# Performance work log

Hardware: AMD Instinct MI355X
Metric: run time of the kernel (lower is better)

## Reference

```python
import jax, jax.numpy as jnp
import numpy as np

B, N, F_IN, F_OUT, E = 2, 8192, 64, 64, 262144
ALPHA = 0.2  # LeakyReLU negative slope


def setup_inputs() -> dict:
    key = jax.random.key(0)
    k1, k2, k3, k4, k5 = jax.random.split(key, 5)
    h = jax.random.normal(k1, (B, N, F_IN), dtype=jnp.float32)
    edge_index = jax.random.randint(k2, (2, E), 0, N, dtype=jnp.int64)
    edge_weight = jax.random.uniform(k3, (E,), dtype=jnp.float32)
    # torch Linear(in,out,bias=False): weight shape (out, in)
    lim_w = float(np.sqrt(1.0 / F_IN))
    W = jax.random.uniform(k4, (F_OUT, F_IN), minval=-lim_w, maxval=lim_w, dtype=jnp.float32)
    # xavier_uniform on (2*out, 1)
    lim_a = float(np.sqrt(6.0 / (2 * F_OUT + 1)))
    a = jax.random.uniform(k5, (2 * F_OUT, 1), minval=-lim_a, maxval=lim_a, dtype=jnp.float32)
    return {"h": h, "W": W, "a": a, "edge_index": edge_index, "edge_weight": edge_weight}


def reference(h, W, a, edge_index, edge_weight):
    src, dst = edge_index[0], edge_index[1]

    def single(hb):  # hb: (N, F_IN)
        Wh = hb @ W.T  # (N, F_OUT)
        edge_h = jnp.concatenate([Wh[src], Wh[dst]], axis=1)  # (E, 2*F_OUT)
        e = jax.nn.leaky_relu((edge_h @ a)[:, 0], negative_slope=ALPHA)  # (E,)
        e = e * edge_weight
        # dense N x N attention, zeros treated as masked (faithful to source)
        attn = jnp.zeros((N, N), dtype=Wh.dtype).at[src, dst].set(e)
        mask = attn == 0
        attn = jnp.where(mask, -jnp.inf, attn)
        attn = jax.nn.softmax(attn, axis=1)
        attn = jnp.where(mask, 0.0, attn)
        h_prime = attn @ Wh  # (N, F_OUT)
        return jax.nn.elu(h_prime)  # concat=True path

    return jax.vmap(single)(h)
```

## Files before the change

### kernel.cpp

```cpp
#include <hip/hip_runtime.h>
#include <hip/hip_bf16.h>
#include <math.h>

#define NN     8192
#define FDIM   64
#define EDGES  262144
#define BATCH  2
#define ALPHA  0.2f

#define NB     256
#define SRCB   32
#define BCAP   1280
#define ROWCAP 128

#define OFF_WH    0u
#define OFF_S1    4194304u
#define OFF_S2    4259840u
#define OFF_OFFS  4325376u
#define OFF_CRS   4456448u
#define OFF_CEW   6553600u

__global__ __launch_bounds__(1024) void stage1_kernel(
    const float* __restrict__ h, const float* __restrict__ W,
    const float* __restrict__ a, const int* __restrict__ ei,
    const float* __restrict__ ew,
    float* __restrict__ Wh, float* __restrict__ s1g, float* __restrict__ s2g,
    unsigned short* __restrict__ offsT, uint2* __restrict__ coarse,
    float* __restrict__ cew) {
  __shared__ float sW[64 * 65];
  __shared__ float sH[64 * 64];
  __shared__ int hist[NB];
  __shared__ int offs[NB];
  int tid = threadIdx.x, lane = tid & 63, w = tid >> 6;
  int blk = blockIdx.x;

  int e = blk * 1024 + tid;
  int s = ei[e], d = ei[EDGES + e];
  int g = s >> 5;
  if (tid < NB) hist[tid] = 0;
  __syncthreads();
  int rank = atomicAdd(&hist[g], 1);
  __syncthreads();
  if (tid < 64) {
    int i0 = tid * 4;
    int c0 = hist[i0], c1 = hist[i0 + 1], c2 = hist[i0 + 2], c3 = hist[i0 + 3];
    int sum = c0 + c1 + c2 + c3;
    int x = sum;
#pragma unroll
    for (int off = 1; off < 64; off <<= 1) {
      int y = __shfl_up(x, off, 64);
      if (tid >= off) x += y;
    }
    int ex = x - sum;
    offs[i0] = ex; offs[i0 + 1] = ex + c0;
    offs[i0 + 2] = ex + c0 + c1; offs[i0 + 3] = ex + c0 + c1 + c2;
  }
  __syncthreads();
  float wgt = ew[e];
  int pos = blk * 1024 + offs[g] + rank;
  coarse[pos] = make_uint2(((unsigned)e << 13) | (unsigned)d, (unsigned)s);
  cew[pos] = wgt;
  if (tid < NB) offsT[tid * 256 + blk] = (unsigned short)offs[tid];

  for (int i = tid; i < 4096; i += 1024) sW[(i >> 6) * 65 + (i & 63)] = W[i];
  int rr = lane >> 4, c4 = lane & 15;
  int nn0 = blk * 64 + w * 4;
  *(float4*)(sH + (w * 4 + rr) * 64 + c4 * 4) =
      *(const float4*)(h + (size_t)(nn0 + rr) * 64 + c4 * 4);
  __syncthreads();

  const float* wp = sW + lane * 65;
  const float* hp = sH + (w * 4) * 64;
  float acc[4] = {0.f, 0.f, 0.f, 0.f};
#pragma unroll 8
  for (int k = 0; k < 64; ++k) {
    float wv = wp[k];
    acc[0] += hp[k] * wv;
    acc[1] += hp[64 + k] * wv;
    acc[2] += hp[128 + k] * wv;
    acc[3] += hp[192 + k] * wv;
  }
  float a1 = a[lane], a2 = a[64 + lane];
#pragma unroll
  for (int r = 0; r < 4; ++r) {
    int nn = nn0 + r;
    Wh[(size_t)nn * 64 + lane] = acc[r];
    float p1 = acc[r] * a1, p2 = acc[r] * a2;
#pragma unroll
    for (int off = 32; off; off >>= 1) {
      p1 += __shfl_xor(p1, off, 64);
      p2 += __shfl_xor(p2, off, 64);
    }
    if (lane == 0) { s1g[nn] = p1; s2g[nn] = p2; }
  }
}

__global__ __launch_bounds__(1024) void stage2_kernel(
    const float* __restrict__ s1g, const float* __restrict__ s2g,
    const unsigned short* __restrict__ offsT, const uint2* __restrict__ coarse,
    const float* __restrict__ cew, const float* __restrict__ Wh,
    float* __restrict__ out) {
  __shared__ uint2 grp[BCAP];
  __shared__ int dstBase[257];
  __shared__ int srcPos[256];
  __shared__ int rhist[SRCB];
  __shared__ int roffs[SRCB];
  __shared__ float s1loc[SRCB];
  __shared__ unsigned bmap[16 * 256];
  int tid = threadIdx.x, lane = tid & 63, w = tid >> 6;
  int blk = blockIdx.x;
  int xcd = blk & 7;
  int b = xcd >> 2;
  int g = (blk >> 3) * 4 + (xcd & 3);
  const float* s2b = s2g + b * NN;
  if (tid < SRCB) {
    rhist[tid] = 0;
    s1loc[tid] = s1g[b * NN + g * SRCB + tid];
  }

  if (tid < 256) {
    int lo = offsT[g * 256 + tid];
    int hi = (g == 255) ? 1024 : offsT[(g + 1) * 256 + tid];
    srcPos[tid] = tid * 1024 + lo;
    dstBase[tid] = hi - lo;
  }
  __syncthreads();
  if (tid < 64) {
    int i0 = tid * 4;
    int c0 = dstBase[i0], c1 = dstBase[i0 + 1], c2 = dstBase[i0 + 2], c3 = dstBase[i0 + 3];
    int sum = c0 + c1 + c2 + c3;
    int x = sum;
#pragma unroll
    for (int off = 1; off < 64; off <<= 1) {
      int y = __shfl_up(x, off, 64);
      if (tid >= off) x += y;
    }
    int ex = x - sum;
    dstBase[i0] = ex; dstBase[i0 + 1] = ex + c0;
    dstBase[i0 + 2] = ex + c0 + c1; dstBase[i0 + 3] = ex + c0 + c1 + c2;
    if (tid == 63) dstBase[256] = x;
  }
  __syncthreads();
  int T = dstBase[256]; if (T > BCAP) T = BCAP;

  unsigned mpk[2]; float mv[2]; int msl[2], mrk[2]; bool mok[2];
#pragma unroll
  for (int j = 0; j < 2; ++j) {
    int i = tid + j * 1024;
    mok[j] = (i < T);
    mpk[j] = 0; mv[j] = 0.f; msl[j] = 0; mrk[j] = 0;
    if (mok[j]) {
      int lo = 0, hi = 255;
#pragma unroll
      for (int st = 0; st < 8; ++st) {
        int mid = (lo + hi + 1) >> 1;
        if (dstBase[mid] <= i) lo = mid; else hi = mid - 1;
      }
      int c = lo, jj = i - dstBase[c];
      uint2 E = coarse[srcPos[c] + jj];
      float wgt = cew[srcPos[c] + jj];
      int dst = (int)(E.x & 0x1FFFu);
      int src = (int)E.y;
      float x = s1loc[src & (SRCB - 1)] + s2b[dst];
      float val = (x > 0.f ? x : ALPHA * x) * wgt;
      mpk[j] = E.x; mv[j] = val; msl[j] = src & (SRCB - 1);
      mrk[j] = atomicAdd(&rhist[msl[j]], 1);
    }
  }
  __syncthreads();
  if (tid < SRCB) {
    int c = rhist[tid];
    int x = c;
#pragma unroll
    for (int off = 1; off < SRCB; off <<= 1) {
      int y = __shfl_up(x, off, 64);
      if (tid >= off) x += y;
    }
    roffs[tid] = x - c;
  }
  __syncthreads();
#pragma unroll
  for (int j = 0; j < 2; ++j)
    if (mok[j]) grp[roffs[msl[j]] + mrk[j]] = make_uint2(mpk[j], __float_as_uint(mv[j]));
  __syncthreads();

  const float* Whb = Wh + (size_t)b * NN * FDIM;
  unsigned* mywords = bmap + w * 256;
  int fg = lane & 15, es = lane >> 4;
  for (int q = 0; q < 2; ++q) {
    int slo = w * 2 + q;
    int beg = roffs[slo];
    int deg = rhist[slo];
    int n = g * SRCB + slo;
    float4 r4 = make_float4(0.f, 0.f, 0.f, 0.f);
    if (deg > 0) {
      float4 acc = make_float4(0.f, 0.f, 0.f, 0.f);
      float inv;
      if (deg <= 64) {
        unsigned k0 = 0; float v0 = 0.f;
        if (lane < deg) { uint2 E = grp[beg + lane]; k0 = E.x; v0 = __uint_as_float(E.y); }
#pragma unroll
        for (int u = 0; u < 4; ++u) mywords[u * 64 + lane] = 0u;
        bool dup = false;
        if (lane < deg) {
          int dst = (int)(k0 & 0x1FFFu);
          unsigned old = atomicOr(&mywords[dst >> 5], 1u << (dst & 31));
          dup = (old >> (dst & 31)) & 1u;
        }
        if (__ballot(dup) != 0ull) {
          for (int j = 0; j < deg; ++j) {
            unsigned q2 = __shfl(k0, j, 64);
            if ((((q2 ^ k0) & 0x1FFFu) == 0u) & (q2 > k0)) v0 = 0.f;
          }
        }
        float4 vv[8];
#pragma unroll
        for (int u = 0; u < 8; ++u) {
          int k = u * 4 + es;
          unsigned key = __shfl(k0, k < deg ? k : 0, 64);
          vv[u] = *((const float4*)(Whb + (size_t)(key & 0x1FFFu) * 64) + fg);
        }
        float p0 = (v0 != 0.f) ? expf(v0) : 0.f;
        float sum = p0;
#pragma unroll
        for (int off = 32; off; off >>= 1) sum += __shfl_xor(sum, off, 64);
        inv = (sum > 0.f) ? 1.f / sum : 0.f;
#pragma unroll
        for (int u = 0; u < 8; ++u) {
          int k = u * 4 + es;
          float p = __shfl(p0, k, 64);
          acc.x += p * vv[u].x; acc.y += p * vv[u].y;
          acc.z += p * vv[u].z; acc.w += p * vv[u].w;
        }
        if (deg > 32) {
          float4 v2[8]; float p2[8];
#pragma unroll
          for (int u = 0; u < 8; ++u) {
            int k = 32 + u * 4 + es;
            unsigned key = __shfl(k0, k < deg ? k : 0, 64);
            p2[u] = __shfl(p0, k, 64);
            v2[u] = *((const float4*)(Whb + (size_t)(key & 0x1FFFu) * 64) + fg);
          }
#pragma unroll
          for (int u = 0; u < 8; ++u) {
            acc.x += p2[u] * v2[u].x; acc.y += p2[u] * v2[u].y;
            acc.z += p2[u] * v2[u].z; acc.w += p2[u] * v2[u].w;
          }
        }
      } else {
        int dg = deg > ROWCAP ? ROWCAP : deg;
        deg = dg;
        unsigned k0 = 0, k1 = 0; float v0 = 0.f, v1 = 0.f;
        { uint2 E = grp[beg + lane]; k0 = E.x; v0 = __uint_as_float(E.y); }
        if (lane + 64 < dg) { uint2 E = grp[beg + lane + 64]; k1 = E.x; v1 = __uint_as_float(E.y); }
        for (int j = 0; j < 64; ++j) {
          unsigned q2 = __shfl(k0, j, 64);
          if ((((q2 ^ k0) & 0x1FFFu) == 0u) & (q2 > k0)) v0 = 0.f;
          if ((((q2 ^ k1) & 0x1FFFu) == 0u) & (q2 > k1)) v1 = 0.f;
        }
        for (int j = 0; j < dg - 64; ++j) {
          unsigned q2 = __shfl(k1, j, 64);
          if ((((q2 ^ k0) & 0x1FFFu) == 0u) & (q2 > k0)) v0 = 0.f;
          if ((((q2 ^ k1) & 0x1FFFu) == 0u) & (q2 > k1)) v1 = 0.f;
        }
        float m = fmaxf((v0 != 0.f) ? v0 : -INFINITY, (v1 != 0.f) ? v1 : -INFINITY);
#pragma unroll
        for (int off = 32; off; off >>= 1) m = fmaxf(m, __shfl_xor(m, off, 64));
        float p0 = (v0 != 0.f) ? expf(v0 - m) : 0.f;
        float p1 = (v1 != 0.f) ? expf(v1 - m) : 0.f;
        float sum = p0 + p1;
#pragma unroll
        for (int off = 32; off; off >>= 1) sum += __shfl_xor(sum, off, 64);
        inv = (sum > 0.f) ? 1.f / sum : 0.f;
        grp[beg + lane].y = __float_as_uint(p0);
        if (lane + 64 < dg) grp[beg + lane + 64].y = __float_as_uint(p1);
        for (int kk = 0; kk < deg; kk += 32) {
          float4 vvv[8]; float pp[8];
#pragma unroll
          for (int u = 0; u < 8; ++u) {
            int k = kk + u * 4 + es;
            int kc = k < deg ? k : deg - 1;
            uint2 E = grp[beg + kc];
            pp[u] = (k < deg) ? __uint_as_float(E.y) : 0.f;
            vvv[u] = *((const float4*)(Whb + (E.x & 0x1FFFu) * 64) + fg);
          }
#pragma unroll
          for (int u = 0; u < 8; ++u) {
            acc.x += pp[u] * vvv[u].x; acc.y += pp[u] * vvv[u].y;
            acc.z += pp[u] * vvv[u].z; acc.w += pp[u] * vvv[u].w;
          }
        }
      }
#pragma unroll
      for (int off = 16; off <= 32; off <<= 1) {
        acc.x += __shfl_xor(acc.x, off, 64);
        acc.y += __shfl_xor(acc.y, off, 64);
        acc.z += __shfl_xor(acc.z, off, 64);
        acc.w += __shfl_xor(acc.w, off, 64);
      }
      r4.x = acc.x * inv; r4.y = acc.y * inv; r4.z = acc.z * inv; r4.w = acc.w * inv;
    }
    if (es == 0) {
      r4.x = r4.x > 0.f ? r4.x : expm1f(r4.x);
      r4.y = r4.y > 0.f ? r4.y : expm1f(r4.y);
      r4.z = r4.z > 0.f ? r4.z : expm1f(r4.z);
      r4.w = r4.w > 0.f ? r4.w : expm1f(r4.w);
      *((float4*)(out + ((size_t)b * NN + n) * 64) + fg) = r4;
    }
  }
}

extern "C" void kernel_launch(void* const* d_in, const int* in_sizes, int n_in,
                              void* d_out, int out_size, void* d_ws, size_t ws_size,
                              hipStream_t stream) {
  const float* h  = (const float*)d_in[0];
  const float* W  = (const float*)d_in[1];
  const float* a  = (const float*)d_in[2];
  const int*   ei = (const int*)d_in[3];
  const float* ew = (const float*)d_in[4];
  float* out = (float*)d_out;

  char* ws = (char*)d_ws;
  float*          Wh     = (float*)(ws + OFF_WH);
  float*          s1     = (float*)(ws + OFF_S1);
  float*          s2     = (float*)(ws + OFF_S2);
  unsigned short* offsT  = (unsigned short*)(ws + OFF_OFFS);
  uint2*          coarse = (uint2*)(ws + OFF_CRS);
  float*          cew    = (float*)(ws + OFF_CEW);

  stage1_kernel<<<256, 1024, 0, stream>>>(h, W, a, ei, ew, Wh, s1, s2, offsT, coarse, cew);
  stage2_kernel<<<BATCH * NB, 1024, 0, stream>>>(s1, s2, offsT, coarse, cew, Wh, out);
}
```

Baseline: 98.49 us.

## Precompute softmax numerators and duplicate flags during edge gather in stage2

Edge records are packed into one 16-byte struct holding the weight, so each edge needs a single load. A segment map replaces the per-edge binary search. Exponentials, per-row sums and duplicate-destination detection are computed during the gather pass using shared atomics, which lets the per-row loop skip the duplicate scan and reduction when a row has no duplicates. The high-degree path drops max subtraction, which risks overflow for large logits, and shared-memory atomics plus a larger dmap array add contention and LDS pressure.

```diff
diff --git a/kernel.cpp b/kernel.cpp
--- a/kernel.cpp
+++ b/kernel.cpp
@@ -18,15 +18,13 @@
 #define OFF_S2    4259840u
 #define OFF_OFFS  4325376u
 #define OFF_CRS   4456448u
-#define OFF_CEW   6553600u
 
 __global__ __launch_bounds__(1024) void stage1_kernel(
     const float* __restrict__ h, const float* __restrict__ W,
     const float* __restrict__ a, const int* __restrict__ ei,
     const float* __restrict__ ew,
     float* __restrict__ Wh, float* __restrict__ s1g, float* __restrict__ s2g,
-    unsigned short* __restrict__ offsT, uint2* __restrict__ coarse,
-    float* __restrict__ cew) {
+    unsigned short* __restrict__ offsT, uint4* __restrict__ coarse4) {
   __shared__ float sW[64 * 65];
   __shared__ float sH[64 * 64];
   __shared__ int hist[NB];
@@ -58,8 +56,8 @@
   __syncthreads();
   float wgt = ew[e];
   int pos = blk * 1024 + offs[g] + rank;
-  coarse[pos] = make_uint2(((unsigned)e << 13) | (unsigned)d, (unsigned)s);
-  cew[pos] = wgt;
+  coarse4[pos] = make_uint4(((unsigned)e << 13) | (unsigned)d, (unsigned)s,
+                            __float_as_uint(wgt), 0u);
   if (tid < NB) offsT[tid * 256 + blk] = (unsigned short)offs[tid];
 
   for (int i = tid; i < 4096; i += 1024) sW[(i >> 6) * 65 + (i & 63)] = W[i];
@@ -97,33 +95,39 @@
 
 __global__ __launch_bounds__(1024) void stage2_kernel(
     const float* __restrict__ s1g, const float* __restrict__ s2g,
-    const unsigned short* __restrict__ offsT, const uint2* __restrict__ coarse,
-    const float* __restrict__ cew, const float* __restrict__ Wh,
-    float* __restrict__ out) {
+    const unsigned short* __restrict__ offsT, const uint4* __restrict__ coarse4,
+    const float* __restrict__ Wh, float* __restrict__ out) {
   __shared__ uint2 grp[BCAP];
   __shared__ int dstBase[257];
   __shared__ int srcPos[256];
+  __shared__ unsigned char segMap[BCAP];
   __shared__ int rhist[SRCB];
   __shared__ int roffs[SRCB];
   __shared__ float s1loc[SRCB];
-  __shared__ unsigned bmap[16 * 256];
+  __shared__ float sumv[SRCB];
+  __shared__ int hasdup[SRCB];
+  __shared__ unsigned dmap[SRCB * 256];
   int tid = threadIdx.x, lane = tid & 63, w = tid >> 6;
   int blk = blockIdx.x;
   int xcd = blk & 7;
   int b = xcd >> 2;
   int g = (blk >> 3) * 4 + (xcd & 3);
   const float* s2b = s2g + b * NN;
+  const float* Whb = Wh + (size_t)b * NN * FDIM;
+  int fg = lane & 15, es = lane >> 4;
+
   if (tid < SRCB) {
-    rhist[tid] = 0;
+    rhist[tid] = 0; sumv[tid] = 0.f; hasdup[tid] = 0;
     s1loc[tid] = s1g[b * NN + g * SRCB + tid];
   }
-
   if (tid < 256) {
     int lo = offsT[g * 256 + tid];
     int hi = (g == 255) ? 1024 : offsT[(g + 1) * 256 + tid];
     srcPos[tid] = tid * 1024 + lo;
     dstBase[tid] = hi - lo;
   }
+#pragma unroll
+  for (int u = 0; u < 8; ++u) dmap[u * 1024 + tid] = 0u;
   __syncthreads();
   if (tid < 64) {
     int i0 = tid * 4;
@@ -142,29 +146,33 @@
   }
   __syncthreads();
   int T = dstBase[256]; if (T > BCAP) T = BCAP;
-
-  unsigned mpk[2]; float mv[2]; int msl[2], mrk[2]; bool mok[2];
+  if (tid < 256) {
+    int lo = dstBase[tid], hi = dstBase[tid + 1];
+    if (hi > BCAP) hi = BCAP;
+    for (int j2 = lo; j2 < hi; ++j2) segMap[j2] = (unsigned char)tid;
+  }
+  __syncthreads();
+
+  unsigned mpk[2]; float mp[2]; int msl[2], mrk[2]; bool mok[2];
 #pragma unroll
   for (int j = 0; j < 2; ++j) {
     int i = tid + j * 1024;
     mok[j] = (i < T);
-    mpk[j] = 0; mv[j] = 0.f; msl[j] = 0; mrk[j] = 0;
+    mpk[j] = 0; mp[j] = 0.f; msl[j] = 0; mrk[j] = 0;
     if (mok[j]) {
-      int lo = 0, hi = 255;
-#pragma unroll
-      for (int st = 0; st < 8; ++st) {
-        int mid = (lo + hi + 1) >> 1;
-        if (dstBase[mid] <= i) lo = mid; else hi = mid - 1;
-      }
-      int c = lo, jj = i - dstBase[c];
-      uint2 E = coarse[srcPos[c] + jj];
-      float wgt = cew[srcPos[c] + jj];
+      int c = segMap[i];
+      int jj = i - dstBase[c];
+      uint4 E = coarse4[srcPos[c] + jj];
       int dst = (int)(E.x & 0x1FFFu);
-      int src = (int)E.y;
-      float x = s1loc[src & (SRCB - 1)] + s2b[dst];
-      float val = (x > 0.f ? x : ALPHA * x) * wgt;
-      mpk[j] = E.x; mv[j] = val; msl[j] = src & (SRCB - 1);
-      mrk[j] = atomicAdd(&rhist[msl[j]], 1);
+      int slo = (int)(E.y & (SRCB - 1));
+      float x = s1loc[slo] + s2b[dst];
+      float val = (x > 0.f ? x : ALPHA * x) * __uint_as_float(E.z);
+      float p = (val != 0.f) ? expf(val) : 0.f;
+      mpk[j] = E.x; mp[j] = p; msl[j] = slo;
+      mrk[j] = atomicAdd(&rhist[slo], 1);
+      atomicAdd(&sumv[slo], p);
+      unsigned old = atomicOr(&dmap[slo * 256 + (dst >> 5)], 1u << (dst & 31));
+      if ((old >> (dst & 31)) & 1u) hasdup[slo] = 1;
     }
   }
   __syncthreads();
@@ -181,12 +189,9 @@
   __syncthreads();
 #pragma unroll
   for (int j = 0; j < 2; ++j)
-    if (mok[j]) grp[roffs[msl[j]] + mrk[j]] = make_uint2(mpk[j], __float_as_uint(mv[j]));
-  __syncthreads();
-
-  const float* Whb = Wh + (size_t)b * NN * FDIM;
-  unsigned* mywords = bmap + w * 256;
-  int fg = lane & 15, es = lane >> 4;
+    if (mok[j]) grp[roffs[msl[j]] + mrk[j]] = make_uint2(mpk[j], __float_as_uint(mp[j]));
+  __syncthreads();
+
   for (int q = 0; q < 2; ++q) {
     int slo = w * 2 + q;
     int beg = roffs[slo];
@@ -197,22 +202,8 @@
       float4 acc = make_float4(0.f, 0.f, 0.f, 0.f);
       float inv;
       if (deg <= 64) {
-        unsigned k0 = 0; float v0 = 0.f;
-        if (lane < deg) { uint2 E = grp[beg + lane]; k0 = E.x; v0 = __uint_as_float(E.y); }
-#pragma unroll
-        for (int u = 0; u < 4; ++u) mywords[u * 64 + lane] = 0u;
-        bool dup = false;
-        if (lane < deg) {
-          int dst = (int)(k0 & 0x1FFFu);
-          unsigned old = atomicOr(&mywords[dst >> 5], 1u << (dst & 31));
-          dup = (old >> (dst & 31)) & 1u;
-        }
-        if (__ballot(dup) != 0ull) {
-          for (int j = 0; j < deg; ++j) {
-            unsigned q2 = __shfl(k0, j, 64);
-            if ((((q2 ^ k0) & 0x1FFFu) == 0u) & (q2 > k0)) v0 = 0.f;
-          }
-        }
+        unsigned k0 = 0; float p0 = 0.f;
+        if (lane < deg) { uint2 E = grp[beg + lane]; k0 = E.x; p0 = __uint_as_float(E.y); }
         float4 vv[8];
 #pragma unroll
         for (int u = 0; u < 8; ++u) {
@@ -220,11 +211,19 @@
           unsigned key = __shfl(k0, k < deg ? k : 0, 64);
           vv[u] = *((const float4*)(Whb + (size_t)(key & 0x1FFFu) * 64) + fg);
         }
-        float p0 = (v0 != 0.f) ? expf(v0) : 0.f;
-        float sum = p0;
-#pragma unroll
-        for (int off = 32; off; off >>= 1) sum += __shfl_xor(sum, off, 64);
-        inv = (sum > 0.f) ? 1.f / sum : 0.f;
+        if (hasdup[slo]) {
+          for (int j = 0; j < deg; ++j) {
+            unsigned q2 = __shfl(k0, j, 64);
+            if ((((q2 ^ k0) & 0x1FFFu) == 0u) & (q2 > k0)) p0 = 0.f;
+          }
+          float sum = p0;
+#pragma unroll
+          for (int off = 32; off; off >>= 1) sum += __shfl_xor(sum, off, 64);
+          inv = (sum > 0.f) ? 1.f / sum : 0.f;
+        } else {
+          float sv = sumv[slo];
+          inv = (sv > 0.f) ? 1.f / sv : 0.f;
+        }
 #pragma unroll
         for (int u = 0; u < 8; ++u) {
           int k = u * 4 + es;
@@ -250,24 +249,19 @@
       } else {
         int dg = deg > ROWCAP ? ROWCAP : deg;
         deg = dg;
-        unsigned k0 = 0, k1 = 0; float v0 = 0.f, v1 = 0.f;
-        { uint2 E = grp[beg + lane]; k0 = E.x; v0 = __uint_as_float(E.y); }
-        if (lane + 64 < dg) { uint2 E = grp[beg + lane + 64]; k1 = E.x; v1 = __uint_as_float(E.y); }
+        unsigned k0 = 0, k1 = 0; float p0 = 0.f, p1 = 0.f;
+        { uint2 E = grp[beg + lane]; k0 = E.x; p0 = __uint_as_float(E.y); }
+        if (lane + 64 < dg) { uint2 E = grp[beg + lane + 64]; k1 = E.x; p1 = __uint_as_float(E.y); }
         for (int j = 0; j < 64; ++j) {
           unsigned q2 = __shfl(k0, j, 64);
-          if ((((q2 ^ k0) & 0x1FFFu) == 0u) & (q2 > k0)) v0 = 0.f;
-          if ((((q2 ^ k1) & 0x1FFFu) == 0u) & (q2 > k1)) v1 = 0.f;
+          if ((((q2 ^ k0) & 0x1FFFu) == 0u) & (q2 > k0)) p0 = 0.f;
+          if ((((q2 ^ k1) & 0x1FFFu) == 0u) & (q2 > k1)) p1 = 0.f;
         }
         for (int j = 0; j < dg - 64; ++j) {
           unsigned q2 = __shfl(k1, j, 64);
-          if ((((q2 ^ k0) & 0x1FFFu) == 0u) & (q2 > k0)) v0 = 0.f;
-          if ((((q2 ^ k1) & 0x1FFFu) == 0u) & (q2 > k1)) v1 = 0.f;
-        }
-        float m = fmaxf((v0 != 0.f) ? v0 : -INFINITY, (v1 != 0.f) ? v1 : -INFINITY);
-#pragma unroll
-        for (int off = 32; off; off >>= 1) m = fmaxf(m, __shfl_xor(m, off, 64));
-        float p0 = (v0 != 0.f) ? expf(v0 - m) : 0.f;
-        float p1 = (v1 != 0.f) ? expf(v1 - m) : 0.f;
+          if ((((q2 ^ k0) & 0x1FFFu) == 0u) & (q2 > k0)) p0 = 0.f;
+          if ((((q2 ^ k1) & 0x1FFFu) == 0u) & (q2 > k1)) p1 = 0.f;
+        }
         float sum = p0 + p1;
 #pragma unroll
         for (int off = 32; off; off >>= 1) sum += __shfl_xor(sum, off, 64);
@@ -321,13 +315,12 @@
   float* out = (float*)d_out;
 
   char* ws = (char*)d_ws;
-  float*          Wh     = (float*)(ws + OFF_WH);
-  float*          s1     = (float*)(ws + OFF_S1);
-  float*          s2     = (float*)(ws + OFF_S2);
-  unsigned short* offsT  = (unsigned short*)(ws + OFF_OFFS);
-  uint2*          coarse = (uint2*)(ws + OFF_CRS);
-  float*          cew    = (float*)(ws + OFF_CEW);
-
-  stage1_kernel<<<256, 1024, 0, stream>>>(h, W, a, ei, ew, Wh, s1, s2, offsT, coarse, cew);
-  stage2_kernel<<<BATCH * NB, 1024, 0, stream>>>(s1, s2, offsT, coarse, cew, Wh, out);
+  float*          Wh      = (float*)(ws + OFF_WH);
+  float*          s1      = (float*)(ws + OFF_S1);
+  float*          s2      = (float*)(ws + OFF_S2);
+  unsigned short* offsT   = (unsigned short*)(ws + OFF_OFFS);
+  uint4*          coarse4 = (uint4*)(ws + OFF_CRS);
+
+  stage1_kernel<<<256, 1024, 0, stream>>>(h, W, a, ei, ew, Wh, s1, s2, offsT, coarse4);
+  stage2_kernel<<<BATCH * NB, 1024, 0, stream>>>(s1, s2, offsT, coarse4, Wh, out);
 }
```

New measurement: 101.1 us. 1.03x slower.
